# Kernel tuning notes

Measured on AMD Instinct MI355X. Metric: run time of the kernel, lower is better.

Reference implementation:

```python
import jax, jax.numpy as jnp
import numpy as np

IN_CH = 256
IN_SIZE = 64
MID_CH = IN_CH // 2
MID_SIZE = IN_SIZE // 2


def setup_inputs() -> dict:
    key = jax.random.key(0)
    k0, k1, k2, k3, k4 = jax.random.split(key, 5)
    x = jax.random.normal(k0, (32, IN_CH, IN_SIZE, IN_SIZE), dtype=jnp.float32)
    # 1x1 conv weights stored as (out_ch, in_ch); bias=False in the module.
    s_ch = 1.0 / np.sqrt(IN_CH)
    s_sz = 1.0 / np.sqrt(IN_SIZE)
    w_left1 = jax.random.normal(k1, (MID_CH, IN_CH), dtype=jnp.float32) * s_ch
    w_left2 = jax.random.normal(k2, (MID_CH, IN_CH), dtype=jnp.float32) * s_ch
    w_right1 = jax.random.normal(k3, (MID_SIZE, IN_SIZE), dtype=jnp.float32) * s_sz
    w_right2 = jax.random.normal(k4, (MID_SIZE, IN_SIZE), dtype=jnp.float32) * s_sz
    return {"x": x, "w_left1": w_left1, "w_left2": w_left2,
            "w_right1": w_right1, "w_right2": w_right2}


def _att(x, w1, w2):
    # x: (b, c, h, w); w1, w2: (m, c) 1x1-conv weights.
    b, c, h, w = x.shape
    x1 = jnp.einsum('mc,bchw->bmhw', w1, x)          # (b, m, h, w)
    x2 = jnp.mean(x1, axis=(2, 3))                    # adaptive avg pool -> (b, m)
    x3 = jnp.einsum('mc,bchw->bmhw', w2, x).reshape(b, -1, h * w)  # (b, m, hw)
    x4 = jnp.einsum('bm,bmn->bn', x2, x3)             # (b, hw)
    x5 = jax.nn.softmax(x4, axis=-1)
    x6 = jax.nn.sigmoid(x5).reshape(b, 1, h, w)
    return x * x6


def reference(x, w_left1, w_left2, w_right1, w_right2):
    # spatial attention on (b, C, H, W)
    sp = _att(x, w_left1, w_left2)
    # channel attention along H: view (b, H, C, W)
    x1 = jnp.transpose(x, (0, 2, 1, 3))
    ch_h = jnp.transpose(_att(x1, w_right1, w_right2), (0, 2, 1, 3))
    # channel attention along W: view (b, W, H, C)
    x2 = jnp.transpose(x, (0, 3, 2, 1))
    ch_w = jnp.transpose(_att(x2, w_right1, w_right2), (0, 3, 2, 1))
    return sp + ch_h + ch_w
```

## Files before the change

kernel.cpp:

```cpp
#include <hip/hip_runtime.h>

#define NB 32
#define NC 256
#define NH 64
#define NW 64
#define HW (NH * NW)

typedef float nfloat4 __attribute__((ext_vector_type(4)));

static constexpr size_t OFF_HSUM = 0;
static constexpr size_t OFF_WSUM = OFF_HSUM + (size_t)NB*NC*NH;
static constexpr size_t OFF_CSUM = OFF_WSUM + (size_t)NB*NC*NW;
static constexpr size_t OFF_VSP  = OFF_CSUM + (size_t)NB*NC;
static constexpr size_t OFF_VH   = OFF_VSP  + (size_t)NB*NC;
static constexpr size_t OFF_VW   = OFF_VH   + (size_t)NB*NH;
static constexpr size_t OFF_SH   = OFF_VW   + (size_t)NB*NW;
static constexpr size_t OFF_SW   = OFF_SH   + (size_t)NB*NC*NW;
static constexpr size_t OFF_PART = OFF_SW   + (size_t)NB*NH*NC;
static constexpr size_t OFF_PSP  = OFF_PART + (size_t)NB*32*HW;
static constexpr size_t OFF_PSH  = OFF_PSP  + (size_t)NB*HW;
static constexpr size_t OFF_PSW  = OFF_PSH  + (size_t)NB*NC*NW;

__global__ __launch_bounds__(256) void k_stats(const float* __restrict__ x,
                                               float* __restrict__ ws) {
    const int bc = blockIdx.x;
    const int t  = threadIdx.x;
    const float4* plane = reinterpret_cast<const float4*>(x) + ((size_t)bc << 10);
    const float4 v0 = plane[t];
    const float4 v1 = plane[t + 256];
    const float4 v2 = plane[t + 512];
    const float4 v3 = plane[t + 768];
    const int h0 = t >> 4;

    float hp0 = v0.x + v0.y + v0.z + v0.w;
    float hp1 = v1.x + v1.y + v1.z + v1.w;
    float hp2 = v2.x + v2.y + v2.z + v2.w;
    float hp3 = v3.x + v3.y + v3.z + v3.w;
    #pragma unroll
    for (int d = 1; d < 16; d <<= 1) {
        hp0 += __shfl_xor(hp0, d);
        hp1 += __shfl_xor(hp1, d);
        hp2 += __shfl_xor(hp2, d);
        hp3 += __shfl_xor(hp3, d);
    }
    if ((t & 15) == 0) {
        float* hdst = ws + OFF_HSUM + (size_t)bc * NH;
        hdst[h0]      = hp0;
        hdst[h0 + 16] = hp1;
        hdst[h0 + 32] = hp2;
        hdst[h0 + 48] = hp3;
    }

    float4 wp;
    wp.x = v0.x + v1.x + v2.x + v3.x;
    wp.y = v0.y + v1.y + v2.y + v3.y;
    wp.z = v0.z + v1.z + v2.z + v3.z;
    wp.w = v0.w + v1.w + v2.w + v3.w;
    __shared__ float4 red4[256];
    red4[t] = wp;
    __syncthreads();
    for (int s2 = 128; s2 >= 16; s2 >>= 1) {
        if (t < s2) {
            red4[t].x += red4[t + s2].x;
            red4[t].y += red4[t + s2].y;
            red4[t].z += red4[t + s2].z;
            red4[t].w += red4[t + s2].w;
        }
        __syncthreads();
    }
    if (t < 16)
        reinterpret_cast<float4*>(ws + OFF_WSUM + (size_t)bc * NW)[t] = red4[t];
    if (t == 0) {
        float s = 0.f;
        #pragma unroll
        for (int i = 0; i < 16; ++i)
            s += red4[i].x + red4[i].y + red4[i].z + red4[i].w;
        ws[OFF_CSUM + bc] = s;
    }
}

__global__ __launch_bounds__(256) void k_vecs(const float* __restrict__ wl1,
                                              const float* __restrict__ wl2,
                                              const float* __restrict__ wr1,
                                              const float* __restrict__ wr2,
                                              float* __restrict__ ws) {
    const int b = blockIdx.x, t = threadIdx.x;
    __shared__ float xbc[256], xbh[64], xbw[64], x2sp[128], th[32], tw[32];
    __shared__ float red[256];

    xbc[t] = ws[OFF_CSUM + (size_t)b * NC + t] * (1.0f / 4096.0f);

    {
        const int h = t & 63, part = t >> 6;
        float s = 0.f;
        const float* hs = ws + OFF_HSUM + ((size_t)b * NC + part * 64) * NH + h;
        for (int c = 0; c < 64; ++c) s += hs[(size_t)c * NH];
        red[t] = s;
        __syncthreads();
        if (t < 64) xbh[t] = (red[t] + red[t + 64] + red[t + 128] + red[t + 192]) * (1.0f / 16384.0f);
        __syncthreads();
    }
    {
        const int w = t & 63, part = t >> 6;
        float s = 0.f;
        const float* wsrc = ws + OFF_WSUM + ((size_t)b * NC + part * 64) * NW + w;
        for (int c = 0; c < 64; ++c) s += wsrc[(size_t)c * NW];
        red[t] = s;
        __syncthreads();
        if (t < 64) xbw[t] = (red[t] + red[t + 64] + red[t + 128] + red[t + 192]) * (1.0f / 16384.0f);
        __syncthreads();
    }

    if (t < 128) {
        float a = 0.f;
        for (int c = 0; c < 256; ++c) a += wl1[t * 256 + c] * xbc[c];
        x2sp[t] = a;
    } else if (t < 160) {
        const int m = t - 128;
        float a = 0.f;
        for (int h = 0; h < 64; ++h) a += wr1[m * 64 + h] * xbh[h];
        th[m] = a;
    } else if (t < 192) {
        const int m = t - 160;
        float a = 0.f;
        for (int h = 0; h < 64; ++h) a += wr1[m * 64 + h] * xbw[h];
        tw[m] = a;
    }
    __syncthreads();

    {
        float a = 0.f;
        for (int m = 0; m < 128; ++m) a += x2sp[m] * wl2[m * 256 + t];
        ws[OFF_VSP + (size_t)b * NC + t] = a;
    }
    if (t < 64) {
        float a = 0.f;
        for (int m = 0; m < 32; ++m) a += th[m] * wr2[m * 64 + t];
        ws[OFF_VH + (size_t)b * NH + t] = a;
    } else if (t < 128) {
        const int w = t - 64;
        float a = 0.f;
        for (int m = 0; m < 32; ++m) a += tw[m] * wr2[m * 64 + w];
        ws[OFF_VW + (size_t)b * NW + w] = a;
    }
}

__global__ __launch_bounds__(256) void k_scores(const float* __restrict__ x,
                                                float* __restrict__ ws) {
    const int t   = threadIdx.x;
    const int blk = blockIdx.x;
    const int b   = blk >> 5;
    const int h0  = t >> 4, w4 = t & 15;

    __shared__ float vh_s[64], vw_s[64], vsp_s[256];
    __shared__ float4 red4[256];

    if (t < 64)       vh_s[t]      = ws[OFF_VH + (size_t)b * NH + t];
    else if (t < 128) vw_s[t - 64] = ws[OFF_VW + (size_t)b * NW + (t - 64)];
    vsp_s[t] = ws[OFF_VSP + (size_t)b * NC + t];
    __syncthreads();

    float4 acc0 = make_float4(0.f,0.f,0.f,0.f);
    float4 acc1 = make_float4(0.f,0.f,0.f,0.f);
    float4 acc2 = make_float4(0.f,0.f,0.f,0.f);
    float4 acc3 = make_float4(0.f,0.f,0.f,0.f);

    for (int p = 0; p < 8; ++p) {
        const int bc = blk * 8 + p;
        const int c  = bc & 255;
        const float4* plane = reinterpret_cast<const float4*>(x) + ((size_t)bc << 10);
        const float4 v0 = plane[t];
        const float4 v1 = plane[t + 256];
        const float4 v2 = plane[t + 512];
        const float4 v3 = plane[t + 768];

        const float4 vwv = reinterpret_cast<const float4*>(vw_s)[w4];
        float hp0 = vwv.x*v0.x + vwv.y*v0.y + vwv.z*v0.z + vwv.w*v0.w;
        float hp1 = vwv.x*v1.x + vwv.y*v1.y + vwv.z*v1.z + vwv.w*v1.w;
        float hp2 = vwv.x*v2.x + vwv.y*v2.y + vwv.z*v2.z + vwv.w*v2.w;
        float hp3 = vwv.x*v3.x + vwv.y*v3.y + vwv.z*v3.z + vwv.w*v3.w;
        #pragma unroll
        for (int d = 1; d < 16; d <<= 1) {
            hp0 += __shfl_xor(hp0, d);
            hp1 += __shfl_xor(hp1, d);
            hp2 += __shfl_xor(hp2, d);
            hp3 += __shfl_xor(hp3, d);
        }
        if (w4 == 0) {
            float* dst = ws + OFF_SW + (size_t)b * NH * NC + c;
            dst[(size_t)(h0)      * NC] = hp0;
            dst[(size_t)(h0 + 16) * NC] = hp1;
            dst[(size_t)(h0 + 32) * NC] = hp2;
            dst[(size_t)(h0 + 48) * NC] = hp3;
        }

        const float a0 = vh_s[h0], a1 = vh_s[h0+16], a2 = vh_s[h0+32], a3 = vh_s[h0+48];
        float4 wp;
        wp.x = a0*v0.x + a1*v1.x + a2*v2.x + a3*v3.x;
        wp.y = a0*v0.y + a1*v1.y + a2*v2.y + a3*v3.y;
        wp.z = a0*v0.z + a1*v1.z + a2*v2.z + a3*v3.z;
        wp.w = a0*v0.w + a1*v1.w + a2*v2.w + a3*v3.w;
        red4[t] = wp;
        __syncthreads();
        for (int s2 = 128; s2 >= 16; s2 >>= 1) {
            if (t < s2) {
                red4[t].x += red4[t + s2].x;
                red4[t].y += red4[t + s2].y;
                red4[t].z += red4[t + s2].z;
                red4[t].w += red4[t + s2].w;
            }
            __syncthreads();
        }
        if (t < 16)
            reinterpret_cast<float4*>(ws + OFF_SH + (size_t)bc * NW)[t] = red4[t];
        __syncthreads();

        const float vc = vsp_s[c];
        acc0.x += vc*v0.x; acc0.y += vc*v0.y; acc0.z += vc*v0.z; acc0.w += vc*v0.w;
        acc1.x += vc*v1.x; acc1.y += vc*v1.y; acc1.z += vc*v1.z; acc1.w += vc*v1.w;
        acc2.x += vc*v2.x; acc2.y += vc*v2.y; acc2.z += vc*v2.z; acc2.w += vc*v2.w;
        acc3.x += vc*v3.x; acc3.y += vc*v3.y; acc3.z += vc*v3.z; acc3.w += vc*v3.w;
    }

    float4* pf4 = reinterpret_cast<float4*>(ws + OFF_PART) +
                  ((size_t)b * 32 + (blk & 31)) * 1024;
    pf4[t]       = acc0;
    pf4[t + 256] = acc1;
    pf4[t + 512] = acc2;
    pf4[t + 768] = acc3;
}

__global__ __launch_bounds__(256) void k_softmax(float* __restrict__ ws) {
    const int blk = blockIdx.x, t = threadIdx.x;
    const int kind = blk >> 5, b = blk & 31;
    __shared__ float red[256];
    __shared__ float4 ssp4[1024];

    if (kind == 0) {
        const float4* part = reinterpret_cast<const float4*>(ws + OFF_PART) +
                             (size_t)b * 32 * 1024;
        #pragma unroll
        for (int j = 0; j < 4; ++j) {
            const int n4 = j * 256 + t;
            float4 a = make_float4(0.f,0.f,0.f,0.f);
            for (int s = 0; s < 32; ++s) {
                const float4 v = part[(size_t)s * 1024 + n4];
                a.x += v.x; a.y += v.y; a.z += v.z; a.w += v.w;
            }
            ssp4[n4] = a;
        }
        __syncthreads();

        float mx = -3.4e38f;
        #pragma unroll
        for (int j = 0; j < 4; ++j) {
            const float4 v = ssp4[j * 256 + t];
            mx = fmaxf(mx, fmaxf(fmaxf(v.x, v.y), fmaxf(v.z, v.w)));
        }
        red[t] = mx;
        __syncthreads();
        for (int s = 128; s > 0; s >>= 1) {
            if (t < s) red[t] = fmaxf(red[t], red[t + s]);
            __syncthreads();
        }
        mx = red[0];
        __syncthreads();

        float sm = 0.f;
        #pragma unroll
        for (int j = 0; j < 4; ++j) {
            const float4 v = ssp4[j * 256 + t];
            sm += expf(v.x - mx) + expf(v.y - mx) + expf(v.z - mx) + expf(v.w - mx);
        }
        red[t] = sm;
        __syncthreads();
        for (int s = 128; s > 0; s >>= 1) {
            if (t < s) red[t] += red[t + s];
            __syncthreads();
        }
        const float inv = 1.0f / red[0];
        float4* dst = reinterpret_cast<float4*>(ws + OFF_PSP + (size_t)b * HW);
        #pragma unroll
        for (int j = 0; j < 4; ++j) {
            const float4 v = ssp4[j * 256 + t];
            float4 o;
            o.x = 1.0f / (1.0f + expf(-(expf(v.x - mx) * inv)));
            o.y = 1.0f / (1.0f + expf(-(expf(v.y - mx) * inv)));
            o.z = 1.0f / (1.0f + expf(-(expf(v.z - mx) * inv)));
            o.w = 1.0f / (1.0f + expf(-(expf(v.w - mx) * inv)));
            dst[j * 256 + t] = o;
        }
        return;
    }

    const float* src;
    float* dst;
    const int N = NC * NW;
    if (kind == 1) { src = ws + OFF_SH + (size_t)b * NC * NW; dst = ws + OFF_PSH + (size_t)b * NC * NW; }
    else           { src = ws + OFF_SW + (size_t)b * NH * NC; dst = ws + OFF_PSW + (size_t)b * NH * NC; }

    float mx = -3.4e38f;
    for (int i = t; i < N; i += 256) mx = fmaxf(mx, src[i]);
    red[t] = mx;
    __syncthreads();
    for (int s = 128; s > 0; s >>= 1) {
        if (t < s) red[t] = fmaxf(red[t], red[t + s]);
        __syncthreads();
    }
    mx = red[0];
    __syncthreads();

    float sm = 0.f;
    for (int i = t; i < N; i += 256) sm += expf(src[i] - mx);
    red[t] = sm;
    __syncthreads();
    for (int s = 128; s > 0; s >>= 1) {
        if (t < s) red[t] += red[t + s];
        __syncthreads();
    }
    const float inv = 1.0f / red[0];
    for (int i = t; i < N; i += 256) {
        const float pr = expf(src[i] - mx) * inv;
        dst[i] = 1.0f / (1.0f + expf(-pr));
    }
}

__global__ __launch_bounds__(256) void k_final(const float* __restrict__ x,
                                               const float* __restrict__ ws,
                                               float* __restrict__ out) {
    const float* psp = ws + OFF_PSP;
    const float* psh = ws + OFF_PSH;
    const float* psw = ws + OFF_PSW;
    nfloat4* out4 = reinterpret_cast<nfloat4*>(out);
    size_t i4 = (size_t)blockIdx.x * 256 + threadIdx.x;
    #pragma unroll 4
    for (int it = 0; it < 16; ++it, i4 += (size_t)2048 * 256) {
        const int w4 = (int)(i4 & 15);
        const int h  = (int)((i4 >> 4) & 63);
        const int c  = (int)((i4 >> 10) & 255);
        const int b  = (int)(i4 >> 18);
        const float4 xv = reinterpret_cast<const float4*>(x)[i4];
        const float4 sp = reinterpret_cast<const float4*>(psp)[((size_t)b << 10) + (h << 4) + w4];
        const float4 sh = reinterpret_cast<const float4*>(psh)[(((size_t)b << 8) + c) * 16 + w4];
        const float  sw = psw[((size_t)b << 14) + (h << 8) + c];
        nfloat4 o;
        o.x = xv.x * (sp.x + sh.x + sw);
        o.y = xv.y * (sp.y + sh.y + sw);
        o.z = xv.z * (sp.z + sh.z + sw);
        o.w = xv.w * (sp.w + sh.w + sw);
        __builtin_nontemporal_store(o, &out4[i4]);
    }
}

extern "C" void kernel_launch(void* const* d_in, const int* in_sizes, int n_in,
                              void* d_out, int out_size, void* d_ws, size_t ws_size,
                              hipStream_t stream) {
    const float* x   = (const float*)d_in[0];
    const float* wl1 = (const float*)d_in[1];
    const float* wl2 = (const float*)d_in[2];
    const float* wr1 = (const float*)d_in[3];
    const float* wr2 = (const float*)d_in[4];
    float* out = (float*)d_out;
    float* ws  = (float*)d_ws;

    k_stats  <<<NB * NC, 256, 0, stream>>>(x, ws);
    k_vecs   <<<NB, 256, 0, stream>>>(wl1, wl2, wr1, wr2, ws);
    k_scores <<<1024, 256, 0, stream>>>(x, ws);
    k_softmax<<<3 * NB, 256, 0, stream>>>(ws);
    k_final  <<<2048, 256, 0, stream>>>(x, ws, out);
}
```

Before: 332.1 us.

## Fuse per-batch vector computation into scores kernel and coarsen stats kernel

The stats kernel now processes 8 channel planes per block and writes per-strip partial row and column sums, not per-channel sums, which shrinks the intermediate write traffic. The small per-batch weight-vector kernel is removed: each scores block recomputes the batch's attention vectors from the partials and weights in shared memory, saving a launch and a global round trip. The cost is redundant matvec work repeated in all 32 blocks per batch, which adds latency before each scores block starts streaming x.

After: 338.6 us. No clear change (+2.0%).

```diff
diff --git a/kernel.cpp b/kernel.cpp
--- a/kernel.cpp
+++ b/kernel.cpp
@@ -20,44 +20,58 @@
 static constexpr size_t OFF_PSP  = OFF_PART + (size_t)NB*32*HW;
 static constexpr size_t OFF_PSH  = OFF_PSP  + (size_t)NB*HW;
 static constexpr size_t OFF_PSW  = OFF_PSH  + (size_t)NB*NC*NW;
-
-__global__ __launch_bounds__(256) void k_stats(const float* __restrict__ x,
-                                               float* __restrict__ ws) {
-    const int bc = blockIdx.x;
-    const int t  = threadIdx.x;
-    const float4* plane = reinterpret_cast<const float4*>(x) + ((size_t)bc << 10);
-    const float4 v0 = plane[t];
-    const float4 v1 = plane[t + 256];
-    const float4 v2 = plane[t + 512];
-    const float4 v3 = plane[t + 768];
-    const int h0 = t >> 4;
-
-    float hp0 = v0.x + v0.y + v0.z + v0.w;
-    float hp1 = v1.x + v1.y + v1.z + v1.w;
-    float hp2 = v2.x + v2.y + v2.z + v2.w;
-    float hp3 = v3.x + v3.y + v3.z + v3.w;
+static constexpr size_t OFF_PARTH= OFF_PSW  + (size_t)NB*NH*NC;
+static constexpr size_t OFF_PARTW= OFF_PARTH+ (size_t)NB*32*64;
+
+__global__ __launch_bounds__(256) void k_stats2(const float* __restrict__ x,
+                                                float* __restrict__ ws) {
+    const int blk = blockIdx.x;
+    const int t   = threadIdx.x;
+    const int b = blk >> 5, strip = blk & 31;
+    const int h0 = t >> 4, w4 = t & 15;
+    const int bc0 = blk * 8;
+
+    float ra0 = 0.f, ra1 = 0.f, ra2 = 0.f, ra3 = 0.f;
+    float4 colacc = make_float4(0.f, 0.f, 0.f, 0.f);
+    float ps[8];
+
+    const float4* base = reinterpret_cast<const float4*>(x) + ((size_t)bc0 << 10);
+    #pragma unroll
+    for (int p = 0; p < 8; ++p) {
+        const float4* plane = base + ((size_t)p << 10);
+        const float4 v0 = plane[t];
+        const float4 v1 = plane[t + 256];
+        const float4 v2 = plane[t + 512];
+        const float4 v3 = plane[t + 768];
+        const float hp0 = v0.x + v0.y + v0.z + v0.w;
+        const float hp1 = v1.x + v1.y + v1.z + v1.w;
+        const float hp2 = v2.x + v2.y + v2.z + v2.w;
+        const float hp3 = v3.x + v3.y + v3.z + v3.w;
+        ps[p] = hp0 + hp1 + hp2 + hp3;
+        ra0 += hp0; ra1 += hp1; ra2 += hp2; ra3 += hp3;
+        colacc.x += v0.x + v1.x + v2.x + v3.x;
+        colacc.y += v0.y + v1.y + v2.y + v3.y;
+        colacc.z += v0.z + v1.z + v2.z + v3.z;
+        colacc.w += v0.w + v1.w + v2.w + v3.w;
+    }
+
     #pragma unroll
     for (int d = 1; d < 16; d <<= 1) {
-        hp0 += __shfl_xor(hp0, d);
-        hp1 += __shfl_xor(hp1, d);
-        hp2 += __shfl_xor(hp2, d);
-        hp3 += __shfl_xor(hp3, d);
-    }
-    if ((t & 15) == 0) {
-        float* hdst = ws + OFF_HSUM + (size_t)bc * NH;
-        hdst[h0]      = hp0;
-        hdst[h0 + 16] = hp1;
-        hdst[h0 + 32] = hp2;
-        hdst[h0 + 48] = hp3;
-    }
-
-    float4 wp;
-    wp.x = v0.x + v1.x + v2.x + v3.x;
-    wp.y = v0.y + v1.y + v2.y + v3.y;
-    wp.z = v0.z + v1.z + v2.z + v3.z;
-    wp.w = v0.w + v1.w + v2.w + v3.w;
+        ra0 += __shfl_xor(ra0, d);
+        ra1 += __shfl_xor(ra1, d);
+        ra2 += __shfl_xor(ra2, d);
+        ra3 += __shfl_xor(ra3, d);
+    }
+    if (w4 == 0) {
+        float* ph = ws + OFF_PARTH + ((size_t)b * 32 + strip) * 64;
+        ph[h0]      = ra0;
+        ph[h0 + 16] = ra1;
+        ph[h0 + 32] = ra2;
+        ph[h0 + 48] = ra3;
+    }
+
     __shared__ float4 red4[256];
-    red4[t] = wp;
+    red4[t] = colacc;
     __syncthreads();
     for (int s2 = 128; s2 >= 16; s2 >>= 1) {
         if (t < s2) {
@@ -69,47 +83,56 @@
         __syncthreads();
     }
     if (t < 16)
-        reinterpret_cast<float4*>(ws + OFF_WSUM + (size_t)bc * NW)[t] = red4[t];
-    if (t == 0) {
+        reinterpret_cast<float4*>(ws + OFF_PARTW + ((size_t)b * 32 + strip) * 64)[t] = red4[t];
+
+    #pragma unroll
+    for (int p = 0; p < 8; ++p) {
+        #pragma unroll
+        for (int d = 1; d < 64; d <<= 1) ps[p] += __shfl_xor(ps[p], d);
+    }
+    __shared__ float wsum8[4][8];
+    const int lane = t & 63, wid = t >> 6;
+    if (lane == 0) {
+        #pragma unroll
+        for (int p = 0; p < 8; ++p) wsum8[wid][p] = ps[p];
+    }
+    __syncthreads();
+    if (t < 8)
+        ws[OFF_CSUM + bc0 + t] = wsum8[0][t] + wsum8[1][t] + wsum8[2][t] + wsum8[3][t];
+}
+
+__global__ __launch_bounds__(256) void k_scores2(const float* __restrict__ x,
+                                                 const float* __restrict__ wl1,
+                                                 const float* __restrict__ wl2,
+                                                 const float* __restrict__ wr1,
+                                                 const float* __restrict__ wr2,
+                                                 float* __restrict__ ws) {
+    const int t   = threadIdx.x;
+    const int blk = blockIdx.x;
+    const int b   = blk >> 5;
+    const int h0  = t >> 4, w4 = t & 15;
+
+    __shared__ float xbc[256], xbh[64], xbw[64], x2sp[128], th_s[32], tw_s[32];
+    __shared__ float red[256];
+    __shared__ float vh_s[64], vw_s[64], vsp_s[256];
+    __shared__ float4 red4[256];
+
+    xbc[t] = ws[OFF_CSUM + (size_t)b * NC + t] * (1.0f / 4096.0f);
+    if (t < 64) {
         float s = 0.f;
-        #pragma unroll
-        for (int i = 0; i < 16; ++i)
-            s += red4[i].x + red4[i].y + red4[i].z + red4[i].w;
-        ws[OFF_CSUM + bc] = s;
-    }
-}
-
-__global__ __launch_bounds__(256) void k_vecs(const float* __restrict__ wl1,
-                                              const float* __restrict__ wl2,
-                                              const float* __restrict__ wr1,
-                                              const float* __restrict__ wr2,
-                                              float* __restrict__ ws) {
-    const int b = blockIdx.x, t = threadIdx.x;
-    __shared__ float xbc[256], xbh[64], xbw[64], x2sp[128], th[32], tw[32];
-    __shared__ float red[256];
-
-    xbc[t] = ws[OFF_CSUM + (size_t)b * NC + t] * (1.0f / 4096.0f);
-
-    {
-        const int h = t & 63, part = t >> 6;
+        const float* ph = ws + OFF_PARTH + (size_t)b * 32 * 64 + t;
+        #pragma unroll 8
+        for (int s2 = 0; s2 < 32; ++s2) s += ph[s2 * 64];
+        xbh[t] = s * (1.0f / 16384.0f);
+    } else if (t < 128) {
+        const int w = t - 64;
         float s = 0.f;
-        const float* hs = ws + OFF_HSUM + ((size_t)b * NC + part * 64) * NH + h;
-        for (int c = 0; c < 64; ++c) s += hs[(size_t)c * NH];
-        red[t] = s;
-        __syncthreads();
-        if (t < 64) xbh[t] = (red[t] + red[t + 64] + red[t + 128] + red[t + 192]) * (1.0f / 16384.0f);
-        __syncthreads();
-    }
-    {
-        const int w = t & 63, part = t >> 6;
-        float s = 0.f;
-        const float* wsrc = ws + OFF_WSUM + ((size_t)b * NC + part * 64) * NW + w;
-        for (int c = 0; c < 64; ++c) s += wsrc[(size_t)c * NW];
-        red[t] = s;
-        __syncthreads();
-        if (t < 64) xbw[t] = (red[t] + red[t + 64] + red[t + 128] + red[t + 192]) * (1.0f / 16384.0f);
-        __syncthreads();
-    }
+        const float* pw = ws + OFF_PARTW + (size_t)b * 32 * 64 + w;
+        #pragma unroll 8
+        for (int s2 = 0; s2 < 32; ++s2) s += pw[s2 * 64];
+        xbw[w] = s * (1.0f / 16384.0f);
+    }
+    __syncthreads();
 
     if (t < 128) {
         float a = 0.f;
@@ -119,45 +142,30 @@
         const int m = t - 128;
         float a = 0.f;
         for (int h = 0; h < 64; ++h) a += wr1[m * 64 + h] * xbh[h];
-        th[m] = a;
+        th_s[m] = a;
     } else if (t < 192) {
         const int m = t - 160;
         float a = 0.f;
         for (int h = 0; h < 64; ++h) a += wr1[m * 64 + h] * xbw[h];
-        tw[m] = a;
+        tw_s[m] = a;
     }
     __syncthreads();
 
     {
         float a = 0.f;
         for (int m = 0; m < 128; ++m) a += x2sp[m] * wl2[m * 256 + t];
-        ws[OFF_VSP + (size_t)b * NC + t] = a;
+        vsp_s[t] = a;
     }
     if (t < 64) {
         float a = 0.f;
-        for (int m = 0; m < 32; ++m) a += th[m] * wr2[m * 64 + t];
-        ws[OFF_VH + (size_t)b * NH + t] = a;
+        for (int m = 0; m < 32; ++m) a += th_s[m] * wr2[m * 64 + t];
+        vh_s[t] = a;
     } else if (t < 128) {
         const int w = t - 64;
         float a = 0.f;
-        for (int m = 0; m < 32; ++m) a += tw[m] * wr2[m * 64 + w];
-        ws[OFF_VW + (size_t)b * NW + w] = a;
-    }
-}
-
-__global__ __launch_bounds__(256) void k_scores(const float* __restrict__ x,
-                                                float* __restrict__ ws) {
-    const int t   = threadIdx.x;
-    const int blk = blockIdx.x;
-    const int b   = blk >> 5;
-    const int h0  = t >> 4, w4 = t & 15;
-
-    __shared__ float vh_s[64], vw_s[64], vsp_s[256];
-    __shared__ float4 red4[256];
-
-    if (t < 64)       vh_s[t]      = ws[OFF_VH + (size_t)b * NH + t];
-    else if (t < 128) vw_s[t - 64] = ws[OFF_VW + (size_t)b * NW + (t - 64)];
-    vsp_s[t] = ws[OFF_VSP + (size_t)b * NC + t];
+        for (int m = 0; m < 32; ++m) a += tw_s[m] * wr2[m * 64 + w];
+        vw_s[w] = a;
+    }
     __syncthreads();
 
     float4 acc0 = make_float4(0.f,0.f,0.f,0.f);
@@ -363,9 +371,8 @@
     float* out = (float*)d_out;
     float* ws  = (float*)d_ws;
 
-    k_stats  <<<NB * NC, 256, 0, stream>>>(x, ws);
-    k_vecs   <<<NB, 256, 0, stream>>>(wl1, wl2, wr1, wr2, ws);
-    k_scores <<<1024, 256, 0, stream>>>(x, ws);
+    k_stats2 <<<1024, 256, 0, stream>>>(x, ws);
+    k_scores2<<<1024, 256, 0, stream>>>(x, wl1, wl2, wr1, wr2, ws);
     k_softmax<<<3 * NB, 256, 0, stream>>>(ws);
     k_final  <<<2048, 256, 0, stream>>>(x, ws, out);
 }
```
